# Kernel tuning notes

Measured on AMD Instinct MI355X. Metric: run time of the kernel, lower is better.

The kernel has to match this reference:

```python
import jax, jax.numpy as jnp
import numpy as np

NEG = -1e6  # mask fill value used by d2l-style masked_softmax


def setup_inputs() -> dict:
    key = jax.random.key(0)
    kq, kk, kv, kl = jax.random.split(key, 4)
    B, Lq, Lk, D = 8, 2048, 2048, 64
    Q = jax.random.normal(kq, (B, Lq, D), dtype=jnp.float32)
    K = jax.random.normal(kk, (B, Lk, D), dtype=jnp.float32)
    V = jax.random.normal(kv, (B, Lk, D), dtype=jnp.float32)
    valid_len = jax.random.randint(kl, (B,), 1, Lk + 1, dtype=jnp.int64)
    return {"Q": Q, "K": K, "V": V, "valid_len": valid_len}


def reference(Q, K, V, valid_len):
    d = Q.shape[-1]
    scale = 1.0 / jnp.sqrt(jnp.asarray(d, dtype=Q.dtype))
    # scores: [B, Lq, Lk]
    S = jnp.einsum('bqd,bkd->bqk', Q, K) * scale
    Lk = K.shape[1]
    # per-batch key-length mask: position j valid iff j < valid_len[b]
    mask = jnp.arange(Lk)[None, None, :] < valid_len[:, None, None]
    S = jnp.where(mask, S, NEG)
    A = jax.nn.softmax(S, axis=-1)
    return jnp.einsum('bqk,bkd->bqd', A, V)
```

## Files before the change

### kernel.cpp

```cpp
#include <hip/hip_runtime.h>
#include <hip/hip_bf16.h>


constexpr int B_  = 8;
constexpr int L_  = 2048;
constexpr int D_  = 64;
constexpr int BQ  = 64;
constexpr int BK  = 64;
constexpr int LDK = 72;
constexpr int NQ  = L_ / BQ;

using bf16x8 = __attribute__((ext_vector_type(8))) __bf16;
using f32x4  = __attribute__((ext_vector_type(4))) float;

__device__ __forceinline__ unsigned pack2(float lo, float hi) {
    __hip_bfloat162 h = __float22bfloat162_rn(make_float2(lo, hi));
    return *(unsigned*)&h;
}
__device__ __forceinline__ int sniff_valid(const int* vl, int b) {
    const int p1 = vl[1];
    return (p1 == 0) ? vl[2 * b] : vl[b];
}

__global__ __launch_bounds__(256, 4) void attn_fwd(
    const float* __restrict__ Q, const float* __restrict__ K,
    const float* __restrict__ V, const int* __restrict__ vl,
    float* __restrict__ O, float* __restrict__ Opart,
    float* __restrict__ lpart, int nsplit, int splitk)
{
    __shared__ __align__(16) unsigned short QsPs[BQ * LDK];
    __shared__ __align__(16) unsigned short Ks[BK * LDK];
    __shared__ __align__(16) unsigned short Vt[D_ * LDK];

    const int id   = blockIdx.x;
    const int b    = id & 7;
    const int rest = id >> 3;
    const int qt   = rest & (NQ - 1);
    const int s    = rest >> 5;
    const int tid  = threadIdx.x;
    const int wave = tid >> 6;
    const int lan  = tid & 15;
    const int quad = (tid >> 4) & 3;

    const int valid  = sniff_valid(vl, b);
    const int kstart = s * splitk;
    if (kstart >= valid) return;
    const int kend   = min(kstart + splitk, valid);
    const int ntiles = (kend - kstart + BK - 1) / BK;

    const float* Kg = K + (size_t)b * L_ * D_;
    const float* Vg = V + (size_t)b * L_ * D_;

    const int krow = tid >> 2, kc0 = (tid & 3) * 16;
    const int vk0  = (tid & 31) * 2, vd0 = (tid >> 5) * 8;

    float4 kr[4], vr[4];
    {
        const float* ks = Kg + (size_t)(kstart + krow) * D_ + kc0;
        #pragma unroll
        for (int p = 0; p < 4; ++p) kr[p] = *(const float4*)(ks + 4 * p);
        const float* vs = Vg + (size_t)(kstart + vk0) * D_ + vd0;
        vr[0] = *(const float4*)(vs);
        vr[1] = *(const float4*)(vs + 4);
        vr[2] = *(const float4*)(vs + D_);
        vr[3] = *(const float4*)(vs + D_ + 4);
    }

    {
        const int row = tid >> 2, c0 = (tid & 3) * 16;
        const float* src = Q + ((size_t)b * L_ + qt * BQ + row) * D_ + c0;
        unsigned us[8];
        #pragma unroll
        for (int p = 0; p < 4; ++p) {
            float4 f = *(const float4*)(src + 4 * p);
            us[2*p]   = pack2(f.x * 0.125f, f.y * 0.125f);
            us[2*p+1] = pack2(f.z * 0.125f, f.w * 0.125f);
        }
        *(uint4*)&QsPs[row * LDK + c0]     = *(uint4*)&us[0];
        *(uint4*)&QsPs[row * LDK + c0 + 8] = *(uint4*)&us[4];
    }
    __syncthreads();

    bf16x8 aq0 = *(const bf16x8*)&QsPs[(wave * 16 + lan) * LDK + quad * 8];
    bf16x8 aq1 = *(const bf16x8*)&QsPs[(wave * 16 + lan) * LDK + 32 + quad * 8];

    f32x4 oacc[4];
    #pragma unroll
    for (int c = 0; c < 4; ++c) oacc[c] = (f32x4){0.f, 0.f, 0.f, 0.f};
    float lsum = 0.f;

    unsigned short* Pw = &QsPs[wave * 16 * LDK];

    for (int t = 0; t < ntiles; ++t) {
        const int kt = kstart + t * BK;
        __syncthreads();

        {
            unsigned us[8];
            #pragma unroll
            for (int p = 0; p < 4; ++p) {
                us[2*p]   = pack2(kr[p].x, kr[p].y);
                us[2*p+1] = pack2(kr[p].z, kr[p].w);
            }
            *(uint4*)&Ks[krow * LDK + kc0]     = *(uint4*)&us[0];
            *(uint4*)&Ks[krow * LDK + kc0 + 8] = *(uint4*)&us[4];
        }
        {
            const float* a = (const float*)&vr[0];
            const float* c = (const float*)&vr[2];
            #pragma unroll
            for (int j = 0; j < 8; ++j)
                *(unsigned*)&Vt[(vd0 + j) * LDK + vk0] = pack2(a[j], c[j]);
        }
        __syncthreads();

        if (t + 1 < ntiles) {
            const int kn = kt + BK;
            const float* ks = Kg + (size_t)(kn + krow) * D_ + kc0;
            #pragma unroll
            for (int p = 0; p < 4; ++p) kr[p] = *(const float4*)(ks + 4 * p);
            const float* vs = Vg + (size_t)(kn + vk0) * D_ + vd0;
            vr[0] = *(const float4*)(vs);
            vr[1] = *(const float4*)(vs + 4);
            vr[2] = *(const float4*)(vs + D_);
            vr[3] = *(const float4*)(vs + D_ + 4);
        }

        #pragma unroll
        for (int c = 0; c < 4; ++c) {
            bf16x8 ak0 = *(const bf16x8*)&Ks[(c*16 + lan) * LDK + quad * 8];
            bf16x8 ak1 = *(const bf16x8*)&Ks[(c*16 + lan) * LDK + 32 + quad * 8];
            f32x4 z = (f32x4){0.f, 0.f, 0.f, 0.f};
            z = __builtin_amdgcn_mfma_f32_16x16x32_bf16(ak0, aq0, z, 0, 0, 0);
            z = __builtin_amdgcn_mfma_f32_16x16x32_bf16(ak1, aq1, z, 0, 0, 0);

            const int kbase = kt + c * 16 + quad * 4;
            float p[4];
            #pragma unroll
            for (int r = 0; r < 4; ++r) {
                p[r] = (kbase + r < valid) ? __expf(z[r]) : 0.f;
                lsum += p[r];
            }
            *(uint2*)&Pw[lan * LDK + c * 16 + quad * 4] =
                make_uint2(pack2(p[0], p[1]), pack2(p[2], p[3]));
        }

        bf16x8 ap0 = *(const bf16x8*)&Pw[lan * LDK + quad * 8];
        bf16x8 ap1 = *(const bf16x8*)&Pw[lan * LDK + 32 + quad * 8];
        #pragma unroll
        for (int c = 0; c < 4; ++c) {
            bf16x8 bv0 = *(const bf16x8*)&Vt[(c*16 + lan) * LDK + quad * 8];
            bf16x8 bv1 = *(const bf16x8*)&Vt[(c*16 + lan) * LDK + 32 + quad * 8];
            oacc[c] = __builtin_amdgcn_mfma_f32_16x16x32_bf16(ap0, bv0, oacc[c], 0, 0, 0);
            oacc[c] = __builtin_amdgcn_mfma_f32_16x16x32_bf16(ap1, bv1, oacc[c], 0, 0, 0);
        }
    }

    lsum += __shfl_xor(lsum, 16);
    lsum += __shfl_xor(lsum, 32);

    const int rowbase = qt * BQ + wave * 16;
    if (nsplit == 1) {
        float inv[4];
        #pragma unroll
        for (int r = 0; r < 4; ++r)
            inv[r] = 1.0f / __shfl(lsum, quad * 4 + r);
        float* Og = O + ((size_t)b * L_ + rowbase) * D_;
        #pragma unroll
        for (int c = 0; c < 4; ++c)
            #pragma unroll
            for (int r = 0; r < 4; ++r)
                Og[(size_t)(quad * 4 + r) * D_ + c * 16 + lan] = oacc[c][r] * inv[r];
    } else {
        float* Og = Opart + ((size_t)s * B_ * L_ + (size_t)b * L_ + rowbase) * D_;
        #pragma unroll
        for (int c = 0; c < 4; ++c)
            #pragma unroll
            for (int r = 0; r < 4; ++r)
                Og[(size_t)(quad * 4 + r) * D_ + c * 16 + lan] = oacc[c][r];
        if (quad == 0)
            lpart[(size_t)s * B_ * L_ + (size_t)b * L_ + rowbase + lan] = lsum;
    }
}

__global__ __launch_bounds__(256) void attn_combine(
    const float* __restrict__ Opart, const float* __restrict__ lpart,
    const int* __restrict__ vl, float* __restrict__ O,
    int nsplit, int splitk)
{
    const int idx = blockIdx.x * 256 + threadIdx.x;
    const int row = idx >> 4;
    const int b   = row >> 11;
    const int off = (idx & 15) * 4;
    const int valid = sniff_valid(vl, b);
    const int ns = min(nsplit, (valid + splitk - 1) / splitk);

    float Lsum = 0.f;
    float4 acc = make_float4(0.f, 0.f, 0.f, 0.f);
    for (int s = 0; s < ns; ++s) {
        Lsum += lpart[s * (B_ * L_) + row];
        float4 o4 = *(const float4*)&Opart[(size_t)s * (B_ * L_ * D_) + (size_t)row * D_ + off];
        acc.x += o4.x; acc.y += o4.y; acc.z += o4.z; acc.w += o4.w;
    }
    const float inv = 1.0f / Lsum;
    acc.x *= inv; acc.y *= inv; acc.z *= inv; acc.w *= inv;
    *(float4*)&O[(size_t)row * D_ + off] = acc;
}

extern "C" void kernel_launch(void* const* d_in, const int* in_sizes, int n_in,
                              void* d_out, int out_size, void* d_ws, size_t ws_size,
                              hipStream_t stream) {
    const float* Q  = (const float*)d_in[0];
    const float* K  = (const float*)d_in[1];
    const float* V  = (const float*)d_in[2];
    const int*   vl = (const int*)d_in[3];
    float* O = (float*)d_out;

    auto need = [](int n) {
        return (size_t)n * (B_ * L_ * D_ + B_ * L_) * sizeof(float);
    };
    int nsplit = 1;
    if      (ws_size >= need(8)) nsplit = 8;
    else if (ws_size >= need(4)) nsplit = 4;
    else if (ws_size >= need(2)) nsplit = 2;
    const int splitk = L_ / nsplit;

    float* Opart = (float*)d_ws;
    float* lpart = Opart + (size_t)nsplit * B_ * L_ * D_;

    attn_fwd<<<dim3(nsplit * B_ * NQ), 256, 0, stream>>>(
        Q, K, V, vl, O, Opart, lpart, nsplit, splitk);
    if (nsplit > 1)
        attn_combine<<<dim3((B_ * L_ * D_ / 4) / 256), 256, 0, stream>>>(
            Opart, lpart, vl, O, nsplit, splitk);
}
```

Baseline: 95.37 us.

## Double query tile per block so each wave reuses K/V tiles over 32 rows

Raises the query tile from 64 to 128 rows so each wave handles two 16-row groups, reusing every staged K and V fragment for twice as many MFMAs. This halves global K/V loads and conversions per query row. Q fragments are now loaded straight from global memory into registers instead of going through shared memory, and P gets its own shared buffer. The cost is more registers and accumulators (occupancy hint dropped from 4 to 3 blocks) and half as many blocks, which may hurt load balance on a GPU with many CUs.

```diff
diff --git a/kernel.cpp b/kernel.cpp
--- a/kernel.cpp
+++ b/kernel.cpp
@@ -5,7 +5,7 @@
 constexpr int B_  = 8;
 constexpr int L_  = 2048;
 constexpr int D_  = 64;
-constexpr int BQ  = 64;
+constexpr int BQ  = 128;
 constexpr int BK  = 64;
 constexpr int LDK = 72;
 constexpr int NQ  = L_ / BQ;
@@ -13,6 +13,8 @@
 using bf16x8 = __attribute__((ext_vector_type(8))) __bf16;
 using f32x4  = __attribute__((ext_vector_type(4))) float;
 
+union frag_u { unsigned u[4]; bf16x8 v; };
+
 __device__ __forceinline__ unsigned pack2(float lo, float hi) {
     __hip_bfloat162 h = __float22bfloat162_rn(make_float2(lo, hi));
     return *(unsigned*)&h;
@@ -22,21 +24,21 @@
     return (p1 == 0) ? vl[2 * b] : vl[b];
 }
 
-__global__ __launch_bounds__(256, 4) void attn_fwd(
+__global__ __launch_bounds__(256, 3) void attn_fwd(
     const float* __restrict__ Q, const float* __restrict__ K,
     const float* __restrict__ V, const int* __restrict__ vl,
     float* __restrict__ O, float* __restrict__ Opart,
     float* __restrict__ lpart, int nsplit, int splitk)
 {
-    __shared__ __align__(16) unsigned short QsPs[BQ * LDK];
     __shared__ __align__(16) unsigned short Ks[BK * LDK];
     __shared__ __align__(16) unsigned short Vt[D_ * LDK];
+    __shared__ __align__(16) unsigned short Ps[4 * 32 * LDK];
 
     const int id   = blockIdx.x;
     const int b    = id & 7;
     const int rest = id >> 3;
     const int qt   = rest & (NQ - 1);
-    const int s    = rest >> 5;
+    const int s    = rest >> 4;
     const int tid  = threadIdx.x;
     const int wave = tid >> 6;
     const int lan  = tid & 15;
@@ -66,30 +68,35 @@
         vr[3] = *(const float4*)(vs + D_ + 4);
     }
 
-    {
-        const int row = tid >> 2, c0 = (tid & 3) * 16;
-        const float* src = Q + ((size_t)b * L_ + qt * BQ + row) * D_ + c0;
-        unsigned us[8];
-        #pragma unroll
-        for (int p = 0; p < 4; ++p) {
-            float4 f = *(const float4*)(src + 4 * p);
-            us[2*p]   = pack2(f.x * 0.125f, f.y * 0.125f);
-            us[2*p+1] = pack2(f.z * 0.125f, f.w * 0.125f);
-        }
-        *(uint4*)&QsPs[row * LDK + c0]     = *(uint4*)&us[0];
-        *(uint4*)&QsPs[row * LDK + c0 + 8] = *(uint4*)&us[4];
-    }
-    __syncthreads();
-
-    bf16x8 aq0 = *(const bf16x8*)&QsPs[(wave * 16 + lan) * LDK + quad * 8];
-    bf16x8 aq1 = *(const bf16x8*)&QsPs[(wave * 16 + lan) * LDK + 32 + quad * 8];
-
-    f32x4 oacc[4];
+    bf16x8 aq[2][2];
     #pragma unroll
-    for (int c = 0; c < 4; ++c) oacc[c] = (f32x4){0.f, 0.f, 0.f, 0.f};
-    float lsum = 0.f;
-
-    unsigned short* Pw = &QsPs[wave * 16 * LDK];
+    for (int g = 0; g < 2; ++g) {
+        const float* qs = Q + ((size_t)b * L_ + qt * BQ + wave * 32 + g * 16 + lan) * D_;
+        float4 q0 = *(const float4*)(qs + quad * 8);
+        float4 q1 = *(const float4*)(qs + quad * 8 + 4);
+        float4 q2 = *(const float4*)(qs + 32 + quad * 8);
+        float4 q3 = *(const float4*)(qs + 32 + quad * 8 + 4);
+        frag_u f0, f1;
+        f0.u[0] = pack2(q0.x * 0.125f, q0.y * 0.125f);
+        f0.u[1] = pack2(q0.z * 0.125f, q0.w * 0.125f);
+        f0.u[2] = pack2(q1.x * 0.125f, q1.y * 0.125f);
+        f0.u[3] = pack2(q1.z * 0.125f, q1.w * 0.125f);
+        f1.u[0] = pack2(q2.x * 0.125f, q2.y * 0.125f);
+        f1.u[1] = pack2(q2.z * 0.125f, q2.w * 0.125f);
+        f1.u[2] = pack2(q3.x * 0.125f, q3.y * 0.125f);
+        f1.u[3] = pack2(q3.z * 0.125f, q3.w * 0.125f);
+        aq[g][0] = f0.v;
+        aq[g][1] = f1.v;
+    }
+
+    f32x4 oacc[2][4];
+    #pragma unroll
+    for (int g = 0; g < 2; ++g)
+        #pragma unroll
+        for (int c = 0; c < 4; ++c) oacc[g][c] = (f32x4){0.f, 0.f, 0.f, 0.f};
+    float lsum[2] = {0.f, 0.f};
+
+    unsigned short* Pw = &Ps[wave * 32 * LDK];
 
     for (int t = 0; t < ntiles; ++t) {
         const int kt = kstart + t * BK;
@@ -130,56 +137,80 @@
         for (int c = 0; c < 4; ++c) {
             bf16x8 ak0 = *(const bf16x8*)&Ks[(c*16 + lan) * LDK + quad * 8];
             bf16x8 ak1 = *(const bf16x8*)&Ks[(c*16 + lan) * LDK + 32 + quad * 8];
-            f32x4 z = (f32x4){0.f, 0.f, 0.f, 0.f};
-            z = __builtin_amdgcn_mfma_f32_16x16x32_bf16(ak0, aq0, z, 0, 0, 0);
-            z = __builtin_amdgcn_mfma_f32_16x16x32_bf16(ak1, aq1, z, 0, 0, 0);
+            f32x4 z0 = (f32x4){0.f, 0.f, 0.f, 0.f};
+            f32x4 z1 = (f32x4){0.f, 0.f, 0.f, 0.f};
+            z0 = __builtin_amdgcn_mfma_f32_16x16x32_bf16(ak0, aq[0][0], z0, 0, 0, 0);
+            z1 = __builtin_amdgcn_mfma_f32_16x16x32_bf16(ak0, aq[1][0], z1, 0, 0, 0);
+            z0 = __builtin_amdgcn_mfma_f32_16x16x32_bf16(ak1, aq[0][1], z0, 0, 0, 0);
+            z1 = __builtin_amdgcn_mfma_f32_16x16x32_bf16(ak1, aq[1][1], z1, 0, 0, 0);
 
             const int kbase = kt + c * 16 + quad * 4;
-            float p[4];
+            float p0[4], p1[4];
             #pragma unroll
             for (int r = 0; r < 4; ++r) {
-                p[r] = (kbase + r < valid) ? __expf(z[r]) : 0.f;
-                lsum += p[r];
+                const bool ok = (kbase + r) < valid;
+                p0[r] = ok ? __expf(z0[r]) : 0.f;
+                p1[r] = ok ? __expf(z1[r]) : 0.f;
+                lsum[0] += p0[r];
+                lsum[1] += p1[r];
             }
             *(uint2*)&Pw[lan * LDK + c * 16 + quad * 4] =
-                make_uint2(pack2(p[0], p[1]), pack2(p[2], p[3]));
-        }
-
-        bf16x8 ap0 = *(const bf16x8*)&Pw[lan * LDK + quad * 8];
-        bf16x8 ap1 = *(const bf16x8*)&Pw[lan * LDK + 32 + quad * 8];
+                make_uint2(pack2(p0[0], p0[1]), pack2(p0[2], p0[3]));
+            *(uint2*)&Pw[(16 + lan) * LDK + c * 16 + quad * 4] =
+                make_uint2(pack2(p1[0], p1[1]), pack2(p1[2], p1[3]));
+        }
+
+        bf16x8 ap[2][2];
+        #pragma unroll
+        for (int g = 0; g < 2; ++g) {
+            ap[g][0] = *(const bf16x8*)&Pw[(g*16 + lan) * LDK + quad * 8];
+            ap[g][1] = *(const bf16x8*)&Pw[(g*16 + lan) * LDK + 32 + quad * 8];
+        }
         #pragma unroll
         for (int c = 0; c < 4; ++c) {
             bf16x8 bv0 = *(const bf16x8*)&Vt[(c*16 + lan) * LDK + quad * 8];
             bf16x8 bv1 = *(const bf16x8*)&Vt[(c*16 + lan) * LDK + 32 + quad * 8];
-            oacc[c] = __builtin_amdgcn_mfma_f32_16x16x32_bf16(ap0, bv0, oacc[c], 0, 0, 0);
-            oacc[c] = __builtin_amdgcn_mfma_f32_16x16x32_bf16(ap1, bv1, oacc[c], 0, 0, 0);
-        }
-    }
-
-    lsum += __shfl_xor(lsum, 16);
-    lsum += __shfl_xor(lsum, 32);
-
-    const int rowbase = qt * BQ + wave * 16;
+            #pragma unroll
+            for (int g = 0; g < 2; ++g) {
+                oacc[g][c] = __builtin_amdgcn_mfma_f32_16x16x32_bf16(ap[g][0], bv0, oacc[g][c], 0, 0, 0);
+                oacc[g][c] = __builtin_amdgcn_mfma_f32_16x16x32_bf16(ap[g][1], bv1, oacc[g][c], 0, 0, 0);
+            }
+        }
+    }
+
+    #pragma unroll
+    for (int g = 0; g < 2; ++g) {
+        lsum[g] += __shfl_xor(lsum[g], 16);
+        lsum[g] += __shfl_xor(lsum[g], 32);
+    }
+
+    const int rowbase = qt * BQ + wave * 32;
     if (nsplit == 1) {
-        float inv[4];
-        #pragma unroll
-        for (int r = 0; r < 4; ++r)
-            inv[r] = 1.0f / __shfl(lsum, quad * 4 + r);
-        float* Og = O + ((size_t)b * L_ + rowbase) * D_;
-        #pragma unroll
-        for (int c = 0; c < 4; ++c)
+        #pragma unroll
+        for (int g = 0; g < 2; ++g) {
+            float inv[4];
             #pragma unroll
             for (int r = 0; r < 4; ++r)
-                Og[(size_t)(quad * 4 + r) * D_ + c * 16 + lan] = oacc[c][r] * inv[r];
+                inv[r] = 1.0f / __shfl(lsum[g], quad * 4 + r);
+            float* Og = O + ((size_t)b * L_ + rowbase + g * 16) * D_;
+            #pragma unroll
+            for (int c = 0; c < 4; ++c)
+                #pragma unroll
+                for (int r = 0; r < 4; ++r)
+                    Og[(size_t)(quad * 4 + r) * D_ + c * 16 + lan] = oacc[g][c][r] * inv[r];
+        }
     } else {
-        float* Og = Opart + ((size_t)s * B_ * L_ + (size_t)b * L_ + rowbase) * D_;
-        #pragma unroll
-        for (int c = 0; c < 4; ++c)
-            #pragma unroll
-            for (int r = 0; r < 4; ++r)
-                Og[(size_t)(quad * 4 + r) * D_ + c * 16 + lan] = oacc[c][r];
-        if (quad == 0)
-            lpart[(size_t)s * B_ * L_ + (size_t)b * L_ + rowbase + lan] = lsum;
+        #pragma unroll
+        for (int g = 0; g < 2; ++g) {
+            float* Og = Opart + ((size_t)s * B_ * L_ + (size_t)b * L_ + rowbase + g * 16) * D_;
+            #pragma unroll
+            for (int c = 0; c < 4; ++c)
+                #pragma unroll
+                for (int r = 0; r < 4; ++r)
+                    Og[(size_t)(quad * 4 + r) * D_ + c * 16 + lan] = oacc[g][c][r];
+            if (quad == 0)
+                lpart[(size_t)s * B_ * L_ + (size_t)b * L_ + rowbase + g * 16 + lan] = lsum[g];
+        }
     }
 }
 
```

Result: faster. 91.30 us (-4.3%).
